# Optimization experiments

Measured on AMD Instinct MI355X. Metric: run time of the kernel, lower is better.

## Reference

```python
import jax, jax.numpy as jnp
import numpy as np
import math

B, S, D, H, FF = 8, 1024, 1024, 16, 4096
DH = D // H
EPS = 1e-5


def _layernorm(x, g, b):
    mu = jnp.mean(x, axis=-1, keepdims=True)
    var = jnp.mean((x - mu) ** 2, axis=-1, keepdims=True)
    return (x - mu) * jax.lax.rsqrt(var + EPS) * g + b


def _gelu_tanh(x):
    c = math.sqrt(2.0 / math.pi)
    return 0.5 * x * (1.0 + jnp.tanh(c * (x + 0.044715 * x ** 3)))


def setup_inputs() -> dict:
    key = jax.random.key(0)
    ks = jax.random.split(key, 8)
    s = lambda d: 1.0 / math.sqrt(d)
    return {
        "x": jax.random.normal(ks[0], (B, S, D), jnp.float32),
        "ln1_g": jnp.ones((D,), jnp.float32),
        "ln1_b": jnp.zeros((D,), jnp.float32),
        "w_qkv": jax.random.normal(ks[1], (3 * D, D), jnp.float32) * s(D),
        "b_qkv": jax.random.normal(ks[2], (3 * D,), jnp.float32) * 0.02,
        "w_o": jax.random.normal(ks[3], (D, D), jnp.float32) * s(D),
        "b_o": jax.random.normal(ks[4], (D,), jnp.float32) * 0.02,
        "ln2_g": jnp.ones((D,), jnp.float32),
        "ln2_b": jnp.zeros((D,), jnp.float32),
        "w1": jax.random.normal(ks[5], (FF, D), jnp.float32) * s(D),
        "b1": jax.random.normal(ks[6], (FF,), jnp.float32) * 0.02,
        "w2": jax.random.normal(ks[7], (D, FF), jnp.float32) * s(FF),
        "b2": jnp.zeros((D,), jnp.float32),
    }


def reference(x, ln1_g, ln1_b, w_qkv, b_qkv, w_o, b_o, ln2_g, ln2_b, w1, b1, w2, b2):
    # --- pre-LN causal self-attention ---
    h = _layernorm(x, ln1_g, ln1_b)
    qkv = h @ w_qkv.T + b_qkv                      # [B,S,3D]
    q, k, v = jnp.split(qkv, 3, axis=-1)
    q = q.reshape(B, S, H, DH)
    k = k.reshape(B, S, H, DH)
    v = v.reshape(B, S, H, DH)
    scores = jnp.einsum("bqhd,bkhd->bhqk", q, k) / math.sqrt(DH)
    causal = jnp.triu(jnp.ones((S, S), jnp.bool_), 1)  # True above diagonal
    scores = jnp.where(causal, -jnp.inf, scores)
    attn = jax.nn.softmax(scores, axis=-1)
    o = jnp.einsum("bhqk,bkhd->bqhd", attn, v).reshape(B, S, D)
    x = x + (o @ w_o.T + b_o)
    # --- FFN ---
    h = _layernorm(x, ln2_g, ln2_b)
    h = _gelu_tanh(h @ w1.T + b1) @ w2.T + b2
    return x + h
```

## Files before the change

kernel.cpp:

```cpp
#include <hip/hip_runtime.h>
#include <math.h>


typedef __bf16 bf16_t;
typedef __bf16 bf16x4 __attribute__((ext_vector_type(4)));
typedef __bf16 bf16x8 __attribute__((ext_vector_type(8)));
typedef float f32x4 __attribute__((ext_vector_type(4)));

__device__ __forceinline__ void async16(const void* g, void* l) {
    __builtin_amdgcn_global_load_lds(
        (const __attribute__((address_space(1))) void*)g,
        (__attribute__((address_space(3))) void*)l,
        16, 0, 0);
}

__device__ __forceinline__ void ln_row(const float* __restrict__ x,
                                       const float* __restrict__ g,
                                       const float* __restrict__ bb,
                                       bf16_t* __restrict__ out, int row) {
    const int tid = threadIdx.x;
    const float4 xv = *(const float4*)(x + row * 1024 + tid * 4);
    float s1 = xv.x + xv.y + xv.z + xv.w;
    float s2 = xv.x * xv.x + xv.y * xv.y + xv.z * xv.z + xv.w * xv.w;
#pragma unroll
    for (int m = 32; m >= 1; m >>= 1) {
        s1 += __shfl_xor(s1, m);
        s2 += __shfl_xor(s2, m);
    }
    __shared__ float r1[4], r2[4];
    const int wid = tid >> 6, lane = tid & 63;
    if (lane == 0) { r1[wid] = s1; r2[wid] = s2; }
    __syncthreads();
    s1 = r1[0] + r1[1] + r1[2] + r1[3];
    s2 = r2[0] + r2[1] + r2[2] + r2[3];
    const float mu = s1 * (1.0f / 1024.0f);
    const float var = s2 * (1.0f / 1024.0f) - mu * mu;
    const float rs = rsqrtf(var + 1e-5f);
    const float4 gv = *(const float4*)(g + tid * 4);
    const float4 bv = *(const float4*)(bb + tid * 4);
    bf16x4 o;
    o[0] = (bf16_t)((xv.x - mu) * rs * gv.x + bv.x);
    o[1] = (bf16_t)((xv.y - mu) * rs * gv.y + bv.y);
    o[2] = (bf16_t)((xv.z - mu) * rs * gv.z + bv.z);
    o[3] = (bf16_t)((xv.w - mu) * rs * gv.w + bv.w);
    *(bf16x4*)(out + row * 1024 + tid * 4) = o;
}

__global__ __launch_bounds__(256) void prep(
    const float* __restrict__ s0, const float* __restrict__ s1,
    const float* __restrict__ s2, const float* __restrict__ s3,
    bf16_t* __restrict__ d0, bf16_t* __restrict__ d1,
    bf16_t* __restrict__ d2, bf16_t* __restrict__ d3,
    const float* __restrict__ x, const float* __restrict__ ln1g,
    const float* __restrict__ ln1b, bf16_t* __restrict__ h) {
    if (blockIdx.x >= 12288) {
        ln_row(x, ln1g, ln1b, h, blockIdx.x - 12288);
        return;
    }
    const int g = blockIdx.x * 256 + threadIdx.x;
    const float* s;
    bf16_t* d;
    int off;
    if (g < 786432)       { s = s0; d = d0; off = g; }
    else if (g < 1048576) { s = s1; d = d1; off = g - 786432; }
    else if (g < 2097152) { s = s2; d = d2; off = g - 1048576; }
    else                  { s = s3; d = d3; off = g - 2097152; }
    const int i = off * 4;
    const float4 v = *(const float4*)(s + i);
    bf16x4 o;
    o[0] = (bf16_t)v.x; o[1] = (bf16_t)v.y; o[2] = (bf16_t)v.z; o[3] = (bf16_t)v.w;
    *(bf16x4*)(d + i) = o;
}

__global__ __launch_bounds__(256) void ln_bf16(const float* __restrict__ x,
                                               const float* __restrict__ g,
                                               const float* __restrict__ bb,
                                               bf16_t* __restrict__ out) {
    ln_row(x, g, bb, out, blockIdx.x);
}

template <int MODE>
__global__ __launch_bounds__(256, 2) void gemm_bt(
    const bf16_t* __restrict__ A, const bf16_t* __restrict__ W,
    const float* __restrict__ bias, const float* __restrict__ resid,
    bf16_t* __restrict__ outb, float* __restrict__ outf,
    bf16_t* __restrict__ vt, int N, int K) {
    __shared__ bf16_t As[128 * 64];
    __shared__ bf16_t Bs[128 * 64];
    const int tid = threadIdx.x;
    const int w = tid >> 6;
    const int lane = tid & 63;
    const int l15 = lane & 15;
    const int quad = lane >> 4;

    const int nbn = N >> 7;
    const int per = 8 * nbn;
    const int lid = blockIdx.x;
    const int bm = (lid / per) * 8 + (lid % per) % 8;
    const int bn = (lid % per) / 8;
    const int m0 = bm * 128;
    const int n0 = bn * 128;
    const int wm = (w & 1) * 64;
    const int wn = (w >> 1) * 64;

    int rr[4], so[4];
#pragma unroll
    for (int q = 0; q < 4; q++) {
        const int c = q * 256 + w * 64 + lane;
        rr[q] = c >> 3;
        so[q] = ((c & 7) ^ (rr[q] & 7)) * 8;
    }
    const bf16_t* pA[4];
    const bf16_t* pB[4];
#pragma unroll
    for (int q = 0; q < 4; q++) {
        pA[q] = A + (size_t)(m0 + rr[q]) * K + so[q];
        pB[q] = W + (size_t)(n0 + rr[q]) * K + so[q];
    }

    f32x4 acc[4][4] = {};

    for (int k0 = 0; k0 < K; k0 += 64) {
#pragma unroll
        for (int q = 0; q < 4; q++) {
            async16(pA[q], As + q * 2048 + w * 512);
            async16(pB[q], Bs + q * 2048 + w * 512);
            pA[q] += 64; pB[q] += 64;
        }
        __syncthreads();

        bf16x8 af[4][2], bfr[4][2];
#pragma unroll
        for (int i = 0; i < 4; i++) {
            const int r = wm + i * 16 + l15;
#pragma unroll
            for (int f = 0; f < 2; f++) {
                const int slot = (f * 4 + quad) ^ (r & 7);
                af[i][f] = *(const bf16x8*)(As + r * 64 + slot * 8);
            }
        }
#pragma unroll
        for (int j = 0; j < 4; j++) {
            const int r = wn + j * 16 + l15;
#pragma unroll
            for (int f = 0; f < 2; f++) {
                const int slot = (f * 4 + quad) ^ (r & 7);
                bfr[j][f] = *(const bf16x8*)(Bs + r * 64 + slot * 8);
            }
        }
#pragma unroll
        for (int i = 0; i < 4; i++)
#pragma unroll
            for (int j = 0; j < 4; j++)
#pragma unroll
                for (int f = 0; f < 2; f++)
                    acc[i][j] = __builtin_amdgcn_mfma_f32_16x16x32_bf16(
                        af[i][f], bfr[j][f], acc[i][j], 0, 0, 0);
        __syncthreads();
    }

#pragma unroll
    for (int i = 0; i < 4; i++) {
#pragma unroll
        for (int j = 0; j < 4; j++) {
            const int col = n0 + wn + j * 16 + l15;
            const float bcol = bias[col];
            const int row0 = m0 + wm + i * 16 + quad * 4;
            float v4[4];
#pragma unroll
            for (int q = 0; q < 4; q++) {
                float v = acc[i][j][q] + bcol;
                if (MODE == 1) {
                    const float u2 = -1.5957691216057308f * (v + 0.044715f * v * v * v);
                    v = v * __builtin_amdgcn_rcpf(1.0f + __expf(u2));
                }
                v4[q] = v;
            }
            if (MODE == 2) {
#pragma unroll
                for (int q = 0; q < 4; q++) {
                    const size_t idx = (size_t)(row0 + q) * N + col;
                    outf[idx] = v4[q] + resid[idx];
                }
            } else if (MODE == 3 && col >= 2048) {
                const int bh = (row0 >> 10) * 16 + ((col - 2048) >> 6);
                const int d = (col - 2048) & 63;
                bf16x4 pk;
#pragma unroll
                for (int q = 0; q < 4; q++) pk[q] = (bf16_t)v4[q];
                *(bf16x4*)(vt + (size_t)bh * 65536 + d * 1024 + (row0 & 1023)) = pk;
            } else {
#pragma unroll
                for (int q = 0; q < 4; q++)
                    outb[(size_t)(row0 + q) * N + col] = (bf16_t)v4[q];
            }
        }
    }
}

__global__ __launch_bounds__(512) void attn_mfma(const bf16_t* __restrict__ qkv,
                                                 const bf16_t* __restrict__ vt,
                                                 bf16_t* __restrict__ o) {
    __shared__ bf16_t Ks[4096];
    __shared__ bf16_t Vs[4096];
    __shared__ bf16_t Ps[8][16][72];
    const int tid = threadIdx.x;
    const int w = tid >> 6;
    const int lane = tid & 63;
    const int l15 = lane & 15;
    const int quad = lane >> 4;
    const int qb = blockIdx.x;
    const int bh = blockIdx.y;
    const int b = bh >> 4, h = bh & 15;

    const int qrow = b * 1024 + qb * 128 + w * 16;
    const int qmaxw = qb * 128 + w * 16 + 15;
    const int ktd = qmaxw >> 6;
    const int kbd = w & 3;

    bf16x8 qf[2];
#pragma unroll
    for (int f = 0; f < 2; f++) {
        bf16x8 t = *(const bf16x8*)(qkv + (size_t)(qrow + l15) * 3072 + h * 64 + f * 32 + quad * 8);
#pragma unroll
        for (int e = 0; e < 8; e++) t[e] = (bf16_t)((float)t[e] * 0.125f);
        qf[f] = t;
    }

    f32x4 Ot[4] = {};
    float mrow = -3.0e38f, lrow = 0.0f;

    const int c0 = w * 64 + lane;
    const int r0 = c0 >> 3, g0 = (((c0 & 7) ^ (r0 & 7))) * 8;

    const bf16_t* kbase = qkv + (size_t)(b * 1024) * 3072 + 1024 + h * 64;
    const bf16_t* vbase = vt + (size_t)bh * 64 * 1024;

    const int ktmax = 2 * qb + 1;
    for (int kt = 0; kt <= ktmax; kt++) {
        async16(kbase + (size_t)(kt * 64 + r0) * 3072 + g0, Ks + w * 512);
        async16(vbase + (size_t)r0 * 1024 + kt * 64 + g0, Vs + w * 512);
        __syncthreads();

        f32x4 sf[4];
#pragma unroll
        for (int kb = 0; kb < 4; kb++) {
            if (kt * 64 + kb * 16 > qmaxw) {
                sf[kb] = (f32x4){-3.0e38f, -3.0e38f, -3.0e38f, -3.0e38f};
                continue;
            }
            const int r = kb * 16 + l15;
            f32x4 acc = {};
#pragma unroll
            for (int f = 0; f < 2; f++) {
                const int seg = (f * 4 + quad) ^ (r & 7);
                const bf16x8 kf = *(const bf16x8*)(Ks + r * 64 + seg * 8);
                acc = __builtin_amdgcn_mfma_f32_16x16x32_bf16(kf, qf[f], acc, 0, 0, 0);
            }
            if (kt == ktd && kb == kbd) {
#pragma unroll
                for (int rr2 = 0; rr2 < 4; rr2++)
                    if (quad * 4 + rr2 > l15) acc[rr2] = -3.0e38f;
            }
            sf[kb] = acc;
        }

        float tmax = -3.0e38f;
#pragma unroll
        for (int kb = 0; kb < 4; kb++)
#pragma unroll
            for (int rr2 = 0; rr2 < 4; rr2++) tmax = fmaxf(tmax, sf[kb][rr2]);
        tmax = fmaxf(tmax, __shfl_xor(tmax, 16));
        tmax = fmaxf(tmax, __shfl_xor(tmax, 32));
        const float mnew = fmaxf(mrow, tmax);
        const float alpha = __expf(mrow - mnew);
        float psum = 0.0f;
#pragma unroll
        for (int kb = 0; kb < 4; kb++) {
            bf16x4 pk;
#pragma unroll
            for (int rr2 = 0; rr2 < 4; rr2++) {
                const float p = __expf(sf[kb][rr2] - mnew);
                psum += p;
                pk[rr2] = (bf16_t)p;
            }
            *(bf16x4*)(&Ps[w][l15][kb * 16 + quad * 4]) = pk;
        }
        psum += __shfl_xor(psum, 16);
        psum += __shfl_xor(psum, 32);
        lrow = lrow * alpha + psum;
        mrow = mnew;
#pragma unroll
        for (int db = 0; db < 4; db++)
#pragma unroll
            for (int rr2 = 0; rr2 < 4; rr2++) Ot[db][rr2] *= alpha;

#pragma unroll
        for (int ks = 0; ks < 2; ks++) {
            if (kt * 64 + ks * 32 > qmaxw) break;
            const bf16x8 pf = *(const bf16x8*)(&Ps[w][l15][ks * 32 + quad * 8]);
#pragma unroll
            for (int db = 0; db < 4; db++) {
                const int d = db * 16 + l15;
                const int seg = (ks * 4 + quad) ^ (d & 7);
                const bf16x8 vf = *(const bf16x8*)(Vs + d * 64 + seg * 8);
                Ot[db] = __builtin_amdgcn_mfma_f32_16x16x32_bf16(vf, pf, Ot[db], 0, 0, 0);
            }
        }
        __syncthreads();
    }

    const float rl = 1.0f / lrow;
#pragma unroll
    for (int db = 0; db < 4; db++) {
        bf16x4 ov;
#pragma unroll
        for (int rr2 = 0; rr2 < 4; rr2++) ov[rr2] = (bf16_t)(Ot[db][rr2] * rl);
        *(bf16x4*)(o + (size_t)(qrow + l15) * 1024 + h * 64 + db * 16 + quad * 4) = ov;
    }
}

extern "C" void kernel_launch(void* const* d_in, const int* in_sizes, int n_in,
                              void* d_out, int out_size, void* d_ws, size_t ws_size,
                              hipStream_t stream) {
    const float* x     = (const float*)d_in[0];
    const float* ln1g  = (const float*)d_in[1];
    const float* ln1b  = (const float*)d_in[2];
    const float* w_qkv = (const float*)d_in[3];
    const float* b_qkv = (const float*)d_in[4];
    const float* w_o   = (const float*)d_in[5];
    const float* b_o   = (const float*)d_in[6];
    const float* ln2g  = (const float*)d_in[7];
    const float* ln2b  = (const float*)d_in[8];
    const float* w1    = (const float*)d_in[9];
    const float* b1    = (const float*)d_in[10];
    const float* w2    = (const float*)d_in[11];
    const float* b2    = (const float*)d_in[12];
    float* out = (float*)d_out;

    char* w = (char*)d_ws;
    bf16_t* wbqkv = (bf16_t*)(w + 0);
    bf16_t* wbo   = (bf16_t*)(w + 6291456);
    bf16_t* wb1   = (bf16_t*)(w + 8388608);
    bf16_t* wb2   = (bf16_t*)(w + 16777216);
    bf16_t* h     = (bf16_t*)(w + 25165824);
    bf16_t* qkv   = (bf16_t*)(w + 41943040);
    bf16_t* ob    = (bf16_t*)(w + 92274688);
    float*  x1    = (float*)(w + 109051904);
    bf16_t* f     = (bf16_t*)(w + 142606336);
    bf16_t* vtb   = (bf16_t*)(w + 142606336);

    prep<<<20480, 256, 0, stream>>>(w_qkv, w_o, w1, w2, wbqkv, wbo, wb1, wb2,
                                    x, ln1g, ln1b, h);
    gemm_bt<3><<<64 * 24, 256, 0, stream>>>(h, wbqkv, b_qkv, nullptr, qkv, nullptr, vtb, 3072, 1024);
    attn_mfma<<<dim3(8, 128), 512, 0, stream>>>(qkv, vtb, ob);
    gemm_bt<2><<<64 * 8, 256, 0, stream>>>(ob, wbo, b_o, x, nullptr, x1, nullptr, 1024, 1024);
    ln_bf16<<<8192, 256, 0, stream>>>(x1, ln2g, ln2b, h);
    gemm_bt<1><<<64 * 32, 256, 0, stream>>>(h, wb1, b1, nullptr, f, nullptr, nullptr, 4096, 1024);
    gemm_bt<2><<<64 * 8, 256, 0, stream>>>(f, wb2, b2, x1, nullptr, out, nullptr, 1024, 4096);
}
```

Baseline: 471.4 us.

## Store residual stream in bf16 and double query rows per attention wave

The intermediate residual x1 is now stored as bf16 instead of fp32. The o-projection GEMM writes bf16 with the fp32 residual added, the second layernorm reads bf16, and the final GEMM adds the bf16 residual. This cuts memory traffic for those stages. Separately, the attention kernel now handles 256 query rows per block (32 per wave, as two 16-row groups), which halves the number of blocks and reuses each loaded K/V tile across twice as many queries. The cost is bf16 rounding on the residual path, which adds error to the output, plus more registers and load imbalance in the causal attention.

```diff
diff --git a/kernel.cpp b/kernel.cpp
--- a/kernel.cpp
+++ b/kernel.cpp
@@ -72,17 +72,45 @@
     *(bf16x4*)(d + i) = o;
 }
 
-__global__ __launch_bounds__(256) void ln_bf16(const float* __restrict__ x,
-                                               const float* __restrict__ g,
-                                               const float* __restrict__ bb,
-                                               bf16_t* __restrict__ out) {
-    ln_row(x, g, bb, out, blockIdx.x);
+__global__ __launch_bounds__(256) void ln_b(const bf16_t* __restrict__ x,
+                                            const float* __restrict__ g,
+                                            const float* __restrict__ bb,
+                                            bf16_t* __restrict__ out) {
+    const int tid = threadIdx.x;
+    const int row = blockIdx.x;
+    const bf16x4 xb = *(const bf16x4*)(x + row * 1024 + tid * 4);
+    const float x0 = (float)xb[0], x1 = (float)xb[1], x2 = (float)xb[2], x3 = (float)xb[3];
+    float s1 = x0 + x1 + x2 + x3;
+    float s2 = x0 * x0 + x1 * x1 + x2 * x2 + x3 * x3;
+#pragma unroll
+    for (int m = 32; m >= 1; m >>= 1) {
+        s1 += __shfl_xor(s1, m);
+        s2 += __shfl_xor(s2, m);
+    }
+    __shared__ float r1[4], r2[4];
+    const int wid = tid >> 6, lane = tid & 63;
+    if (lane == 0) { r1[wid] = s1; r2[wid] = s2; }
+    __syncthreads();
+    s1 = r1[0] + r1[1] + r1[2] + r1[3];
+    s2 = r2[0] + r2[1] + r2[2] + r2[3];
+    const float mu = s1 * (1.0f / 1024.0f);
+    const float var = s2 * (1.0f / 1024.0f) - mu * mu;
+    const float rs = rsqrtf(var + 1e-5f);
+    const float4 gv = *(const float4*)(g + tid * 4);
+    const float4 bv = *(const float4*)(bb + tid * 4);
+    bf16x4 o;
+    o[0] = (bf16_t)((x0 - mu) * rs * gv.x + bv.x);
+    o[1] = (bf16_t)((x1 - mu) * rs * gv.y + bv.y);
+    o[2] = (bf16_t)((x2 - mu) * rs * gv.z + bv.z);
+    o[3] = (bf16_t)((x3 - mu) * rs * gv.w + bv.w);
+    *(bf16x4*)(out + row * 1024 + tid * 4) = o;
 }
 
 template <int MODE>
 __global__ __launch_bounds__(256, 2) void gemm_bt(
     const bf16_t* __restrict__ A, const bf16_t* __restrict__ W,
-    const float* __restrict__ bias, const float* __restrict__ resid,
+    const float* __restrict__ bias, const float* __restrict__ residf,
+    const bf16_t* __restrict__ residb,
     bf16_t* __restrict__ outb, float* __restrict__ outf,
     bf16_t* __restrict__ vt, int N, int K) {
     __shared__ bf16_t As[128 * 64];
@@ -176,11 +204,17 @@
                 }
                 v4[q] = v;
             }
-            if (MODE == 2) {
+            if (MODE == 4) {
 #pragma unroll
                 for (int q = 0; q < 4; q++) {
                     const size_t idx = (size_t)(row0 + q) * N + col;
-                    outf[idx] = v4[q] + resid[idx];
+                    outb[idx] = (bf16_t)(v4[q] + residf[idx]);
+                }
+            } else if (MODE == 5) {
+#pragma unroll
+                for (int q = 0; q < 4; q++) {
+                    const size_t idx = (size_t)(row0 + q) * N + col;
+                    outf[idx] = v4[q] + (float)residb[idx];
                 }
             } else if (MODE == 3 && col >= 2048) {
                 const int bh = (row0 >> 10) * 16 + ((col - 2048) >> 6);
@@ -203,7 +237,7 @@
                                                  bf16_t* __restrict__ o) {
     __shared__ bf16_t Ks[4096];
     __shared__ bf16_t Vs[4096];
-    __shared__ bf16_t Ps[8][16][72];
+    __shared__ bf16_t Ps[8][32][72];
     const int tid = threadIdx.x;
     const int w = tid >> 6;
     const int lane = tid & 63;
@@ -213,22 +247,22 @@
     const int bh = blockIdx.y;
     const int b = bh >> 4, h = bh & 15;
 
-    const int qrow = b * 1024 + qb * 128 + w * 16;
-    const int qmaxw = qb * 128 + w * 16 + 15;
-    const int ktd = qmaxw >> 6;
-    const int kbd = w & 3;
-
-    bf16x8 qf[2];
-#pragma unroll
-    for (int f = 0; f < 2; f++) {
-        bf16x8 t = *(const bf16x8*)(qkv + (size_t)(qrow + l15) * 3072 + h * 64 + f * 32 + quad * 8);
-#pragma unroll
-        for (int e = 0; e < 8; e++) t[e] = (bf16_t)((float)t[e] * 0.125f);
-        qf[f] = t;
-    }
-
-    f32x4 Ot[4] = {};
-    float mrow = -3.0e38f, lrow = 0.0f;
+    const int qrow = b * 1024 + qb * 256 + w * 32;
+
+    bf16x8 qf[2][2];
+#pragma unroll
+    for (int g = 0; g < 2; g++)
+#pragma unroll
+        for (int f = 0; f < 2; f++) {
+            bf16x8 t = *(const bf16x8*)(qkv + (size_t)(qrow + g * 16 + l15) * 3072 + h * 64 + f * 32 + quad * 8);
+#pragma unroll
+            for (int e = 0; e < 8; e++) t[e] = (bf16_t)((float)t[e] * 0.125f);
+            qf[g][f] = t;
+        }
+
+    f32x4 Ot[2][4] = {};
+    float mrow[2] = {-3.0e38f, -3.0e38f};
+    float lrow[2] = {0.0f, 0.0f};
 
     const int c0 = w * 64 + lane;
     const int r0 = c0 >> 3, g0 = (((c0 & 7) ^ (r0 & 7))) * 8;
@@ -236,87 +270,98 @@
     const bf16_t* kbase = qkv + (size_t)(b * 1024) * 3072 + 1024 + h * 64;
     const bf16_t* vbase = vt + (size_t)bh * 64 * 1024;
 
-    const int ktmax = 2 * qb + 1;
+    const int ktmax = 4 * qb + 3;
     for (int kt = 0; kt <= ktmax; kt++) {
         async16(kbase + (size_t)(kt * 64 + r0) * 3072 + g0, Ks + w * 512);
         async16(vbase + (size_t)r0 * 1024 + kt * 64 + g0, Vs + w * 512);
         __syncthreads();
 
-        f32x4 sf[4];
-#pragma unroll
-        for (int kb = 0; kb < 4; kb++) {
-            if (kt * 64 + kb * 16 > qmaxw) {
-                sf[kb] = (f32x4){-3.0e38f, -3.0e38f, -3.0e38f, -3.0e38f};
-                continue;
-            }
-            const int r = kb * 16 + l15;
-            f32x4 acc = {};
-#pragma unroll
-            for (int f = 0; f < 2; f++) {
-                const int seg = (f * 4 + quad) ^ (r & 7);
-                const bf16x8 kf = *(const bf16x8*)(Ks + r * 64 + seg * 8);
-                acc = __builtin_amdgcn_mfma_f32_16x16x32_bf16(kf, qf[f], acc, 0, 0, 0);
-            }
-            if (kt == ktd && kb == kbd) {
-#pragma unroll
-                for (int rr2 = 0; rr2 < 4; rr2++)
-                    if (quad * 4 + rr2 > l15) acc[rr2] = -3.0e38f;
-            }
-            sf[kb] = acc;
-        }
-
-        float tmax = -3.0e38f;
-#pragma unroll
-        for (int kb = 0; kb < 4; kb++)
-#pragma unroll
-            for (int rr2 = 0; rr2 < 4; rr2++) tmax = fmaxf(tmax, sf[kb][rr2]);
-        tmax = fmaxf(tmax, __shfl_xor(tmax, 16));
-        tmax = fmaxf(tmax, __shfl_xor(tmax, 32));
-        const float mnew = fmaxf(mrow, tmax);
-        const float alpha = __expf(mrow - mnew);
-        float psum = 0.0f;
-#pragma unroll
-        for (int kb = 0; kb < 4; kb++) {
-            bf16x4 pk;
-#pragma unroll
-            for (int rr2 = 0; rr2 < 4; rr2++) {
-                const float p = __expf(sf[kb][rr2] - mnew);
-                psum += p;
-                pk[rr2] = (bf16_t)p;
-            }
-            *(bf16x4*)(&Ps[w][l15][kb * 16 + quad * 4]) = pk;
-        }
-        psum += __shfl_xor(psum, 16);
-        psum += __shfl_xor(psum, 32);
-        lrow = lrow * alpha + psum;
-        mrow = mnew;
-#pragma unroll
-        for (int db = 0; db < 4; db++)
-#pragma unroll
-            for (int rr2 = 0; rr2 < 4; rr2++) Ot[db][rr2] *= alpha;
-
-#pragma unroll
-        for (int ks = 0; ks < 2; ks++) {
-            if (kt * 64 + ks * 32 > qmaxw) break;
-            const bf16x8 pf = *(const bf16x8*)(&Ps[w][l15][ks * 32 + quad * 8]);
-#pragma unroll
-            for (int db = 0; db < 4; db++) {
-                const int d = db * 16 + l15;
-                const int seg = (ks * 4 + quad) ^ (d & 7);
-                const bf16x8 vf = *(const bf16x8*)(Vs + d * 64 + seg * 8);
-                Ot[db] = __builtin_amdgcn_mfma_f32_16x16x32_bf16(vf, pf, Ot[db], 0, 0, 0);
+#pragma unroll
+        for (int g = 0; g < 2; g++) {
+            const int qmaxw = qb * 256 + w * 32 + g * 16 + 15;
+            if (kt * 64 > qmaxw) continue;
+            const int ktd = qmaxw >> 6;
+            const int kbd = (2 * w + g) & 3;
+
+            f32x4 sf[4];
+#pragma unroll
+            for (int kb = 0; kb < 4; kb++) {
+                if (kt * 64 + kb * 16 > qmaxw) {
+                    sf[kb] = (f32x4){-3.0e38f, -3.0e38f, -3.0e38f, -3.0e38f};
+                    continue;
+                }
+                const int r = kb * 16 + l15;
+                f32x4 acc = {};
+#pragma unroll
+                for (int f = 0; f < 2; f++) {
+                    const int seg = (f * 4 + quad) ^ (r & 7);
+                    const bf16x8 kf = *(const bf16x8*)(Ks + r * 64 + seg * 8);
+                    acc = __builtin_amdgcn_mfma_f32_16x16x32_bf16(kf, qf[g][f], acc, 0, 0, 0);
+                }
+                if (kt == ktd && kb == kbd) {
+#pragma unroll
+                    for (int rr2 = 0; rr2 < 4; rr2++)
+                        if (quad * 4 + rr2 > l15) acc[rr2] = -3.0e38f;
+                }
+                sf[kb] = acc;
+            }
+
+            float tmax = -3.0e38f;
+#pragma unroll
+            for (int kb = 0; kb < 4; kb++)
+#pragma unroll
+                for (int rr2 = 0; rr2 < 4; rr2++) tmax = fmaxf(tmax, sf[kb][rr2]);
+            tmax = fmaxf(tmax, __shfl_xor(tmax, 16));
+            tmax = fmaxf(tmax, __shfl_xor(tmax, 32));
+            const float mnew = fmaxf(mrow[g], tmax);
+            const float alpha = __expf(mrow[g] - mnew);
+            float psum = 0.0f;
+#pragma unroll
+            for (int kb = 0; kb < 4; kb++) {
+                bf16x4 pk;
+#pragma unroll
+                for (int rr2 = 0; rr2 < 4; rr2++) {
+                    const float p = __expf(sf[kb][rr2] - mnew);
+                    psum += p;
+                    pk[rr2] = (bf16_t)p;
+                }
+                *(bf16x4*)(&Ps[w][g * 16 + l15][kb * 16 + quad * 4]) = pk;
+            }
+            psum += __shfl_xor(psum, 16);
+            psum += __shfl_xor(psum, 32);
+            lrow[g] = lrow[g] * alpha + psum;
+            mrow[g] = mnew;
+#pragma unroll
+            for (int db = 0; db < 4; db++)
+#pragma unroll
+                for (int rr2 = 0; rr2 < 4; rr2++) Ot[g][db][rr2] *= alpha;
+
+#pragma unroll
+            for (int ks = 0; ks < 2; ks++) {
+                if (kt * 64 + ks * 32 > qmaxw) break;
+                const bf16x8 pf = *(const bf16x8*)(&Ps[w][g * 16 + l15][ks * 32 + quad * 8]);
+#pragma unroll
+                for (int db = 0; db < 4; db++) {
+                    const int d = db * 16 + l15;
+                    const int seg = (ks * 4 + quad) ^ (d & 7);
+                    const bf16x8 vf = *(const bf16x8*)(Vs + d * 64 + seg * 8);
+                    Ot[g][db] = __builtin_amdgcn_mfma_f32_16x16x32_bf16(vf, pf, Ot[g][db], 0, 0, 0);
+                }
             }
         }
         __syncthreads();
     }
 
-    const float rl = 1.0f / lrow;
-#pragma unroll
-    for (int db = 0; db < 4; db++) {
-        bf16x4 ov;
-#pragma unroll
-        for (int rr2 = 0; rr2 < 4; rr2++) ov[rr2] = (bf16_t)(Ot[db][rr2] * rl);
-        *(bf16x4*)(o + (size_t)(qrow + l15) * 1024 + h * 64 + db * 16 + quad * 4) = ov;
+#pragma unroll
+    for (int g = 0; g < 2; g++) {
+        const float rl = 1.0f / lrow[g];
+#pragma unroll
+        for (int db = 0; db < 4; db++) {
+            bf16x4 ov;
+#pragma unroll
+            for (int rr2 = 0; rr2 < 4; rr2++) ov[rr2] = (bf16_t)(Ot[g][db][rr2] * rl);
+            *(bf16x4*)(o + (size_t)(qrow + g * 16 + l15) * 1024 + h * 64 + db * 16 + quad * 4) = ov;
+        }
     }
 }
 
@@ -346,16 +391,16 @@
     bf16_t* h     = (bf16_t*)(w + 25165824);
     bf16_t* qkv   = (bf16_t*)(w + 41943040);
     bf16_t* ob    = (bf16_t*)(w + 92274688);
-    float*  x1    = (float*)(w + 109051904);
+    bf16_t* x1b   = (bf16_t*)(w + 109051904);
     bf16_t* f     = (bf16_t*)(w + 142606336);
     bf16_t* vtb   = (bf16_t*)(w + 142606336);
 
     prep<<<20480, 256, 0, stream>>>(w_qkv, w_o, w1, w2, wbqkv, wbo, wb1, wb2,
                                     x, ln1g, ln1b, h);
-    gemm_bt<3><<<64 * 24, 256, 0, stream>>>(h, wbqkv, b_qkv, nullptr, qkv, nullptr, vtb, 3072, 1024);
-    attn_mfma<<<dim3(8, 128), 512, 0, stream>>>(qkv, vtb, ob);
-    gemm_bt<2><<<64 * 8, 256, 0, stream>>>(ob, wbo, b_o, x, nullptr, x1, nullptr, 1024, 1024);
-    ln_bf16<<<8192, 256, 0, stream>>>(x1, ln2g, ln2b, h);
-    gemm_bt<1><<<64 * 32, 256, 0, stream>>>(h, wb1, b1, nullptr, f, nullptr, nullptr, 4096, 1024);
-    gemm_bt<2><<<64 * 8, 256, 0, stream>>>(f, wb2, b2, x1, nullptr, out, nullptr, 1024, 4096);
-}
+    gemm_bt<3><<<64 * 24, 256, 0, stream>>>(h, wbqkv, b_qkv, nullptr, nullptr, qkv, nullptr, vtb, 3072, 1024);
+    attn_mfma<<<dim3(4, 128), 512, 0, stream>>>(qkv, vtb, ob);
+    gemm_bt<4><<<64 * 8, 256, 0, stream>>>(ob, wbo, b_o, x, nullptr, x1b, nullptr, nullptr, 1024, 1024);
+    ln_b<<<8192, 256, 0, stream>>>(x1b, ln2g, ln2b, h);
+    gemm_bt<1><<<64 * 32, 256, 0, stream>>>(h, wb1, b1, nullptr, nullptr, f, nullptr, nullptr, 4096, 1024);
+    gemm_bt<5><<<64 * 8, 256, 0, stream>>>(f, wb2, b2, nullptr, x1b, nullptr, out, nullptr, 1024, 4096);
+}
```

Result: faster. 438.0 us (-7.1%).
